# Kernel optimization log

Hardware: AMD Instinct MI355X
Metric: run time of the kernel (lower is better)

The kernel has to match this reference:

```python
import jax, jax.numpy as jnp
import numpy as np

VOCAB, EMB = 32000, 1024
HID, NLAYERS = 1024, 2
T, B, S = 64, 128, 128


def setup_inputs() -> dict:
    key = jax.random.key(0)
    ks = jax.random.split(key, 16)
    s = 1.0 / np.sqrt(HID)
    inp = {
        "input": jax.random.randint(ks[0], (T, B), 0, VOCAB),
        "h": jax.random.normal(ks[1], (NLAYERS, B, HID), jnp.float32),
        "H": jax.random.normal(ks[2], (S, B, HID), jnp.float32),
        "emb": jax.random.normal(ks[3], (VOCAB, EMB), jnp.float32) * 0.02,
        "w_ih": jax.random.uniform(ks[4], (NLAYERS, 3 * HID, EMB), jnp.float32, -s, s),
        "w_hh": jax.random.uniform(ks[5], (NLAYERS, 3 * HID, HID), jnp.float32, -s, s),
        "b_ih": jax.random.uniform(ks[6], (NLAYERS, 3 * HID), jnp.float32, -s, s),
        "b_hh": jax.random.uniform(ks[7], (NLAYERS, 3 * HID), jnp.float32, -s, s),
        "L1": jax.random.uniform(ks[8], (HID, HID), jnp.float32, -s, s),
        "L2": jax.random.uniform(ks[9], (HID, 2 * HID), jnp.float32, -s, s),
    }
    return inp


def _gru_cell(x, hprev, w_ih, w_hh, b_ih, b_hh):
    # x: (B, in), hprev: (B, HID); torch GRUCell gate order: r, z, n
    gi = x @ w_ih.T + b_ih          # (B, 3H)
    gh = hprev @ w_hh.T + b_hh      # (B, 3H)
    i_r, i_z, i_n = jnp.split(gi, 3, axis=-1)
    h_r, h_z, h_n = jnp.split(gh, 3, axis=-1)
    r = jax.nn.sigmoid(i_r + h_r)
    z = jax.nn.sigmoid(i_z + h_z)
    n = jnp.tanh(i_n + r * h_n)
    return (1.0 - z) * n + z * hprev


def reference(input, h, H, emb, w_ih, w_hh, b_ih, b_hh, L1, L2):
    embed = emb[input]                  # (T, B, EMB)
    Hc = jnp.transpose(H, (1, 0, 2))    # (B, S, HID)

    def step(hcarry, e):
        # stacked GRU cells
        hs = []
        o = e
        for i in range(NLAYERS):
            hi = _gru_cell(o, hcarry[i], w_ih[i], w_hh[i], b_ih[i], b_hh[i])
            hs.append(hi)
            o = hi
        hn = jnp.stack(hs)              # (L, B, HID)
        # global attention
        q1 = o @ L1.T                   # (B, HID)
        a = jax.nn.softmax(jnp.einsum('bsh,bh->bs', Hc, q1), axis=1)
        c = jnp.einsum('bs,bsh->bh', a, Hc)
        out = jnp.tanh(jnp.concatenate([c, o], axis=1) @ L2.T)
        return hn, out

    h_final, output = jax.lax.scan(step, h, embed)
    return output, h_final
```

## Files before the change

kernel.cpp:

```cpp
#include <hip/hip_runtime.h>

#define T_STEPS 64
#define BATCH   128
#define HID     1024
#define H3      3072
#define EMBD    1024
#define SLEN    128
#define BH      (BATCH * HID)

typedef __attribute__((ext_vector_type(8))) short short8;
typedef __attribute__((ext_vector_type(4))) float f32x4;

__device__ __forceinline__ unsigned short f2bf(float x) {
    unsigned int u = __float_as_uint(x);
    unsigned int r = (u + 0x7fffu + ((u >> 16) & 1u)) >> 16;
    return (unsigned short)r;
}
__device__ __forceinline__ float bf2f(unsigned short h) {
    return __uint_as_float(((unsigned int)h) << 16);
}
__device__ __forceinline__ unsigned int pk(unsigned short a, unsigned short b) {
    return (unsigned int)a | ((unsigned int)b << 16);
}
__device__ __forceinline__ void cvt8(const float4& x, const float4& y,
                                     uint4& H, uint4& L) {
    unsigned short h0 = f2bf(x.x), h1 = f2bf(x.y), h2 = f2bf(x.z), h3 = f2bf(x.w);
    unsigned short h4 = f2bf(y.x), h5 = f2bf(y.y), h6 = f2bf(y.z), h7 = f2bf(y.w);
    unsigned short l0 = f2bf(x.x - bf2f(h0)), l1 = f2bf(x.y - bf2f(h1));
    unsigned short l2 = f2bf(x.z - bf2f(h2)), l3 = f2bf(x.w - bf2f(h3));
    unsigned short l4 = f2bf(y.x - bf2f(h4)), l5 = f2bf(y.y - bf2f(h5));
    unsigned short l6 = f2bf(y.z - bf2f(h6)), l7 = f2bf(y.w - bf2f(h7));
    H = make_uint4(pk(h0,h1), pk(h2,h3), pk(h4,h5), pk(h6,h7));
    L = make_uint4(pk(l0,l1), pk(l2,l3), pk(l4,l5), pk(l6,l7));
}
__device__ __forceinline__ float sigf(float x) {
    return 1.f / (1.f + __expf(-x));
}

#define MF(A, B, ACC) ACC = __builtin_amdgcn_mfma_f32_16x16x32_bf16(A, B, ACC, 0, 0, 0)
#define TRI(AH, AL, WH, WL, ACC)  MF(AH, WL, ACC); MF(AL, WH, ACC); MF(AH, WH, ACC);

__global__ __launch_bounds__(256) void conv_planes_k(
    const float* __restrict__ src, short* __restrict__ hi, short* __restrict__ lo)
{
    const long i8 = (long)blockIdx.x * 256 + threadIdx.x;
    float4 x = ((const float4*)src)[i8 * 2];
    float4 y = ((const float4*)src)[i8 * 2 + 1];
    uint4 H, L; cvt8(x, y, H, L);
    ((uint4*)hi)[i8] = H; ((uint4*)lo)[i8] = L;
}

__global__ __launch_bounds__(256) void conv_cat_k(
    const float* __restrict__ wih1, const float* __restrict__ whh1,
    short* __restrict__ hi, short* __restrict__ lo)
{
    const long i8 = (long)blockIdx.x * 256 + threadIdx.x;
    const int k8 = (int)(i8 & 255);
    const long row = i8 >> 8;
    const int k = k8 * 8;
    const float* s = (k < 1024) ? (wih1 + row * 1024 + k) : (whh1 + row * 1024 + (k - 1024));
    float4 x = ((const float4*)s)[0];
    float4 y = ((const float4*)s)[1];
    uint4 H, L; cvt8(x, y, H, L);
    ((uint4*)hi)[i8] = H; ((uint4*)lo)[i8] = L;
}

__global__ __launch_bounds__(256) void conv_gather_k(
    const float* __restrict__ emb, const int* __restrict__ input,
    short* __restrict__ hi, short* __restrict__ lo)
{
    const long i8 = (long)blockIdx.x * 256 + threadIdx.x;
    const int c8 = (int)(i8 & 127);
    const long row = i8 >> 7;
    const float* s = emb + (size_t)input[row] * 1024 + c8 * 8;
    float4 x = ((const float4*)s)[0];
    float4 y = ((const float4*)s)[1];
    uint4 H, L; cvt8(x, y, H, L);
    ((uint4*)hi)[i8] = H; ((uint4*)lo)[i8] = L;
}

template<int MODE, bool CONCAT, bool WLO>
__global__ __launch_bounds__(256, 2) void gemm_big(
    const short* __restrict__ A1h, const short* __restrict__ A1l,
    const short* __restrict__ A2h, const short* __restrict__ A2l,
    const short* __restrict__ Wh,  const short* __restrict__ Wl,
    int K, int nn,
    const float* __restrict__ bias,
    float* __restrict__ outf, short* __restrict__ outh, short* __restrict__ outl,
    int ldo)
{
    extern __shared__ short sm[];
    short* Asm = sm;
    short* Wsm = sm + 16384;
    const int tid = threadIdx.x;
    const int wv = tid >> 6, l = tid & 63;
    const int mq = wv >> 1, nq = wv & 1;
    const int gl = l >> 4, r16 = l & 15;

    const int cpx = gridDim.x >> 3;
    const int id = blockIdx.x;
    const int swz = (id & 7) * cpx + (id >> 3);
    const int bm = swz / nn, bn = swz % nn;
    const long Rbase = (long)bm * 128;
    const int  Cbase = bn * 128;

    const int lda = CONCAT ? (K >> 1) : K;
    const int NC = K >> 5;
    const int NCh = NC >> 1;

    const short *aP1[4], *aP2[4], *wP[4];
    int slda[4];
    #pragma unroll
    for (int j = 0; j < 4; ++j) {
        const int s = tid + j * 256;
        const int pl = s >> 9, sp = s & 511;
        const int row = ((sp >> 6) << 4) | (sp & 15);
        const int kg = (sp >> 4) & 3;
        slda[j] = s * 8;
        const short* a1 = pl ? A1l : A1h;
        aP1[j] = a1 + (Rbase + row) * (long)lda + kg * 8;
        if (CONCAT) {
            const short* a2 = pl ? A2l : A2h;
            aP2[j] = a2 + (Rbase + row) * (long)lda + kg * 8;
        } else aP2[j] = aP1[j];
        const short* wp = pl ? Wl : Wh;
        wP[j] = wp + ((long)Cbase + row) * (long)K + kg * 8;
    }

    f32x4 acc[4][4];
    #pragma unroll
    for (int i = 0; i < 4; ++i)
        #pragma unroll
        for (int j = 0; j < 4; ++j) acc[i][j] = (f32x4)0.f;

    short8 rA[4], rW[4];
    auto LOADC = [&](int c) {
        const bool p1 = !CONCAT || (c < NCh);
        const long ko = p1 ? (long)c * 32 : (long)c * 32 - (K >> 1);
        #pragma unroll
        for (int j = 0; j < 4; ++j) {
            rA[j] = *(const short8*)((p1 ? aP1[j] : aP2[j]) + ko);
            rW[j] = *(const short8*)(wP[j] + (long)c * 32);
        }
    };
    auto STORE = [&](int c) {
        const int b = (c & 1) << 13;
        #pragma unroll
        for (int j = 0; j < 4; ++j) {
            *(short8*)(Asm + b + slda[j]) = rA[j];
            *(short8*)(Wsm + b + slda[j]) = rW[j];
        }
    };

    LOADC(0); STORE(0); LOADC(1);
    __syncthreads();

    for (int c = 0; c < NC; ++c) {
        const int b = (c & 1) << 13;
        short8 ah[4], al[4], wh[4], wl[4];
        #pragma unroll
        for (int f = 0; f < 4; ++f) {
            const short* ab = Asm + b + ((mq * 4 + f) * 64 + l) * 8;
            ah[f] = *(const short8*)ab;
            al[f] = *(const short8*)(ab + 4096);
            const short* wb = Wsm + b + ((nq * 4 + f) * 64 + l) * 8;
            wh[f] = *(const short8*)wb;
            if (!WLO) wl[f] = *(const short8*)(wb + 4096);
        }
        if (c + 1 < NC) STORE(c + 1);
        if (c + 2 < NC) LOADC(c + 2);
        #pragma unroll
        for (int mf = 0; mf < 4; ++mf)
            #pragma unroll
            for (int nf = 0; nf < 4; ++nf) {
                if constexpr (WLO) {
                    MF(al[mf], wh[nf], acc[mf][nf]);
                    MF(ah[mf], wh[nf], acc[mf][nf]);
                } else {
                    TRI(ah[mf], al[mf], wh[nf], wl[nf], acc[mf][nf]);
                }
            }
        __syncthreads();
    }

    #pragma unroll
    for (int mf = 0; mf < 4; ++mf) {
        #pragma unroll
        for (int reg = 0; reg < 4; ++reg) {
            const long R = Rbase + mq * 64 + mf * 16 + gl * 4 + reg;
            #pragma unroll
            for (int nf = 0; nf < 4; ++nf) {
                const int col = Cbase + nq * 64 + nf * 16 + r16;
                float v = acc[mf][nf][reg];
                if constexpr (MODE == 0) {
                    outf[R * (long)ldo + col] = v + bias[col];
                } else if constexpr (MODE == 1) {
                    const unsigned short hi = f2bf(v), lo = f2bf(v - bf2f(hi));
                    outh[R * (long)ldo + col] = (short)hi;
                    outl[R * (long)ldo + col] = (short)lo;
                } else {
                    outf[R * (long)ldo + col] = tanhf(v);
                }
            }
        }
    }
}

template<int MODE>
__device__ __forceinline__ void gru_core(
    int bm, int bj,
    const short* __restrict__ A1h, const short* __restrict__ A1l,
    const short* __restrict__ A2h, const short* __restrict__ A2l,
    const short* __restrict__ Wh,  const short* __restrict__ Wl,
    const float* __restrict__ bias, const float* __restrict__ bias2,
    const float* __restrict__ gi, const float* __restrict__ hprev,
    float* __restrict__ outf, short* __restrict__ outh, short* __restrict__ outl)
{
    extern __shared__ short sm[];
    constexpr int P = 3;
    constexpr int K = (MODE == 2) ? 1024 : 2048;
    constexpr int NC = K >> 6;
    constexpr int NCh = NC >> 1;
    const int ABUF = 8192, WBUF = P * 2048;
    short* Asm = sm;
    short* Wsm = sm + 2 * ABUF;
    const int tid = threadIdx.x;
    const int wv = tid >> 6, l = tid & 63;
    const int gl = l >> 4, r16 = l & 15;

    const short *a1hP[2], *a1lP[2], *a2hP[2], *a2lP[2];
    int aLds[2];
    #pragma unroll
    for (int i = 0; i < 2; ++i) {
        const int s = tid + i * 256;
        const int row = ((s >> 6) & 3) * 16 + (s & 15);
        const int kg  = ((s >> 8) << 2) | ((s >> 4) & 3);
        const long r = (long)bm * 64 + row;
        a1hP[i] = A1h + r * HID + kg * 8;
        a1lP[i] = A1l + r * HID + kg * 8;
        if (MODE == 3) {
            a2hP[i] = A2h + r * HID + kg * 8;
            a2lP[i] = A2l + r * HID + kg * 8;
        } else { a2hP[i] = a1hP[i]; a2lP[i] = a1lP[i]; }
        aLds[i] = s * 8;
    }
    const bool doW = tid < P * 64;
    const short *whP[2], *wlP[2];
    int wLds[2] = {0, 0};
    if (doW) {
        #pragma unroll
        for (int i = 0; i < 2; ++i) {
            const int s = tid + i * P * 64;
            const int kcw = s / (P * 64);
            const int rem = s - kcw * (P * 64);
            const int p = rem >> 6, ll = rem & 63;
            const int jr = ll & 15, g = ll >> 4;
            const int kg = kcw * 4 + g;
            const long grow = (long)(p << 10) + bj * 16 + jr;
            whP[i] = Wh + grow * (long)K + kg * 8;
            wlP[i] = Wl + grow * (long)K + kg * 8;
            wLds[i] = s * 8;
        }
    }

    constexpr int NACC = (MODE == 3) ? 4 : 3;
    f32x4 acc[NACC];
    #pragma unroll
    for (int i = 0; i < NACC; ++i) acc[i] = (f32x4)0.f;

    auto wloNeed = [&](int c) -> bool { return (MODE == 3) && (c < NCh); };

    short8 rAh[2], rAl[2], rWh[2], rWl[2];
    auto LOADC = [&](int c) {
        const bool part1 = (MODE == 2) || (c < NCh);
        const long ko = part1 ? (long)c * 64 : (long)c * 64 - (K >> 1);
        #pragma unroll
        for (int i = 0; i < 2; ++i) {
            rAh[i] = *(const short8*)((part1 ? a1hP[i] : a2hP[i]) + ko);
            rAl[i] = *(const short8*)((part1 ? a1lP[i] : a2lP[i]) + ko);
        }
        if (doW) {
            const bool wl = wloNeed(c);
            #pragma unroll
            for (int i = 0; i < 2; ++i) {
                rWh[i] = *(const short8*)(whP[i] + (long)c * 64);
                if (wl) rWl[i] = *(const short8*)(wlP[i] + (long)c * 64);
            }
        }
    };
    auto STORE = [&](int c) {
        const int b = c & 1;
        #pragma unroll
        for (int i = 0; i < 2; ++i) {
            *(short8*)(Asm + b * ABUF + aLds[i]) = rAh[i];
            *(short8*)(Asm + b * ABUF + 4096 + aLds[i]) = rAl[i];
        }
        if (doW) {
            const bool wl = wloNeed(c);
            #pragma unroll
            for (int i = 0; i < 2; ++i) {
                *(short8*)(Wsm + b * WBUF + wLds[i]) = rWh[i];
                if (wl) *(short8*)(Wsm + b * WBUF + P * 1024 + wLds[i]) = rWl[i];
            }
        }
    };

    LOADC(0); STORE(0); LOADC(1);
    __syncthreads();

    for (int c = 0; c < NC; ++c) {
        const int b = c & 1;
        const bool wl = wloNeed(c);
        short8 fah[2], fal[2], fwh[2][P], fwl[2][P];
        #pragma unroll
        for (int kc = 0; kc < 2; ++kc) {
            const short* ab = Asm + b * ABUF + (kc * 256 + wv * 64 + l) * 8;
            fah[kc] = *(const short8*)ab;
            fal[kc] = *(const short8*)(ab + 4096);
            #pragma unroll
            for (int p = 0; p < P; ++p) {
                const short* wb = Wsm + b * WBUF + (kc * (P * 64) + p * 64 + l) * 8;
                fwh[kc][p] = *(const short8*)wb;
                if (wl) fwl[kc][p] = *(const short8*)(wb + P * 1024);
            }
        }
        if (c + 1 < NC) STORE(c + 1);
        if (c + 2 < NC) LOADC(c + 2);
        #pragma unroll
        for (int kc = 0; kc < 2; ++kc) {
            if constexpr (MODE == 3) {
                if (c < NCh) {
                    TRI(fah[kc], fal[kc], fwh[kc][0], fwl[kc][0], acc[0]);
                    TRI(fah[kc], fal[kc], fwh[kc][1], fwl[kc][1], acc[1]);
                    TRI(fah[kc], fal[kc], fwh[kc][2], fwl[kc][2], acc[2]);
                } else {
                    MF(fal[kc], fwh[kc][0], acc[0]); MF(fah[kc], fwh[kc][0], acc[0]);
                    MF(fal[kc], fwh[kc][1], acc[1]); MF(fah[kc], fwh[kc][1], acc[1]);
                    MF(fal[kc], fwh[kc][2], acc[3]); MF(fah[kc], fwh[kc][2], acc[3]);
                }
            } else {
                #pragma unroll
                for (int p = 0; p < P; ++p) {
                    MF(fal[kc], fwh[kc][p], acc[p]); MF(fah[kc], fwh[kc][p], acc[p]);
                }
            }
        }
        __syncthreads();
    }

    const int jc = bj * 16 + r16;
    #pragma unroll
    for (int reg = 0; reg < 4; ++reg) {
        const long R = (long)bm * 64 + wv * 16 + gl * 4 + reg;
        float h;
        if constexpr (MODE == 2) {
            const float* orow = gi + R * H3;
            const float rr = sigf(orow[jc] + acc[0][reg] + bias[jc]);
            const float zz = sigf(orow[HID + jc] + acc[1][reg] + bias[HID + jc]);
            const float nn = tanhf(orow[2 * HID + jc] + rr * (acc[2][reg] + bias[2 * HID + jc]));
            h = (1.f - zz) * nn + zz * hprev[R * HID + jc];
        } else {
            const float rr = sigf(acc[0][reg] + bias[jc] + bias2[jc]);
            const float zz = sigf(acc[1][reg] + bias[HID + jc] + bias2[HID + jc]);
            const float nn = tanhf(acc[2][reg] + bias[2 * HID + jc] +
                                   rr * (acc[3][reg] + bias2[2 * HID + jc]));
            h = (1.f - zz) * nn + zz * hprev[R * HID + jc];
        }
        outf[R * HID + jc] = h;
        const unsigned short hb = f2bf(h), lb = f2bf(h - bf2f(hb));
        outh[R * HID + jc] = (short)hb;
        outl[R * HID + jc] = (short)lb;
    }
}

struct StepP {
    const short* hih; const short* hil;
    const float* h_in; const float* gi0;
    const short* whh0h;
    const short* wcath; const short* wcatl;
    const float* b_hh0; const float* b_ih1; const float* b_hh1;
    float* h0f; float* h1f;
    short* h0ah; short* h0al; short* h1ah; short* h1al;
};

__global__ __launch_bounds__(256) void step_k(int t, StepP P)
{
    const int id = blockIdx.x;
    const int xcd = id & 7, sub = (id >> 3) & 7, top = id >> 6;
    const int role = top >> 1, bm = top & 1;
    const int bj = xcd * 8 + sub;

    if (role == 0) {
        if (t >= T_STEPS) return;
        const short* a1h = t ? P.h0ah + (size_t)(t - 1) * BH : P.hih;
        const short* a1l = t ? P.h0al + (size_t)(t - 1) * BH : P.hil;
        gru_core<2>(bm, bj, a1h, a1l, nullptr, nullptr,
                    P.whh0h, nullptr, P.b_hh0, nullptr,
                    P.gi0 + (size_t)t * BATCH * H3,
                    t ? P.h0f + (size_t)((t - 1) & 1) * BH : P.h_in,
                    P.h0f + (size_t)(t & 1) * BH,
                    P.h0ah + (size_t)t * BH, P.h0al + (size_t)t * BH);
    } else {
        if (t < 1) return;
        const int s = t - 1;
        const short* a2h = s ? P.h1ah + (size_t)(s - 1) * BH : P.hih + BH;
        const short* a2l = s ? P.h1al + (size_t)(s - 1) * BH : P.hil + BH;
        gru_core<3>(bm, bj,
                    P.h0ah + (size_t)s * BH, P.h0al + (size_t)s * BH, a2h, a2l,
                    P.wcath, P.wcatl, P.b_ih1, P.b_hh1,
                    nullptr,
                    s ? P.h1f + (size_t)((s - 1) & 1) * BH : P.h_in + BH,
                    P.h1f + (size_t)(s & 1) * BH,
                    P.h1ah + (size_t)s * BH, P.h1al + (size_t)s * BH);
    }
}

__global__ __launch_bounds__(256) void scores_k(
    const short* __restrict__ Qh, const short* __restrict__ Ql,
    const short* __restrict__ Hh, const short* __restrict__ Hl,
    float* __restrict__ Pall)
{
    extern __shared__ short sm[];
    short* Asm = sm;
    short* Wsm = sm + 8192;
    const int b = blockIdx.x, tid = threadIdx.x;
    const int wv = tid >> 6, l = tid & 63;
    const int gl = l >> 4, cc = l & 15;

    const int arow = ((tid >> 6) & 3) * 16 + (tid & 15);
    const int ag   = (tid >> 4) & 3;
    const short* qhp = Qh + ((long)arow * BATCH + b) * HID + ag * 8;
    const short* qlp = Ql + ((long)arow * BATCH + b) * HID + ag * 8;
    const int aLds = tid * 8;

    const short *whp[2], *wlp[2]; int wLds[2];
    #pragma unroll
    for (int i = 0; i < 2; ++i) {
        const int s = tid + i * 256;
        const int srow = ((s >> 6) & 7) * 16 + (s & 15);
        const int sg   = (s >> 4) & 3;
        whp[i] = Hh + ((long)srow * BATCH + b) * HID + sg * 8;
        wlp[i] = Hl + ((long)srow * BATCH + b) * HID + sg * 8;
        wLds[i] = s * 8;
    }

    f32x4 acc[8];
    #pragma unroll
    for (int i = 0; i < 8; ++i) acc[i] = (f32x4)0.f;

    short8 rAh, rAl, rWh[2], rWl[2];
    auto LOADC = [&](int c) {
        rAh = *(const short8*)(qhp + c * 32);
        rAl = *(const short8*)(qlp + c * 32);
        #pragma unroll
        for (int i = 0; i < 2; ++i) {
            rWh[i] = *(const short8*)(whp[i] + c * 32);
            rWl[i] = *(const short8*)(wlp[i] + c * 32);
        }
    };
    auto STORE = [&](int c) {
        const int bb = c & 1;
        *(short8*)(Asm + bb * 4096 + aLds) = rAh;
        *(short8*)(Asm + bb * 4096 + 2048 + aLds) = rAl;
        #pragma unroll
        for (int i = 0; i < 2; ++i) {
            *(short8*)(Wsm + bb * 8192 + wLds[i]) = rWh[i];
            *(short8*)(Wsm + bb * 8192 + 4096 + wLds[i]) = rWl[i];
        }
    };

    LOADC(0); STORE(0); LOADC(1);
    __syncthreads();
    for (int c = 0; c < 32; ++c) {
        const int bb = c & 1;
        const short* abp = Asm + bb * 4096 + (wv * 64 + l) * 8;
        short8 ah = *(const short8*)abp;
        short8 al = *(const short8*)(abp + 2048);
        if (c + 1 < 32) STORE(c + 1);
        if (c + 2 < 32) LOADC(c + 2);
        #pragma unroll
        for (int jt = 0; jt < 8; ++jt) {
            const short* wbp = Wsm + bb * 8192 + (jt * 64 + l) * 8;
            short8 wh = *(const short8*)wbp;
            short8 wl = *(const short8*)(wbp + 4096);
            TRI(ah, al, wh, wl, acc[jt]);
        }
        __syncthreads();
    }

    #pragma unroll
    for (int reg = 0; reg < 4; ++reg) {
        float m = acc[0][reg];
        #pragma unroll
        for (int jt = 1; jt < 8; ++jt) m = fmaxf(m, acc[jt][reg]);
        #pragma unroll
        for (int off = 1; off < 16; off <<= 1) m = fmaxf(m, __shfl_xor(m, off));
        float e[8], ssum = 0.f;
        #pragma unroll
        for (int jt = 0; jt < 8; ++jt) { e[jt] = __expf(acc[jt][reg] - m); ssum += e[jt]; }
        #pragma unroll
        for (int off = 1; off < 16; off <<= 1) ssum += __shfl_xor(ssum, off);
        const float inv = 1.f / ssum;
        const int t = wv * 16 + gl * 4 + reg;
        #pragma unroll
        for (int jt = 0; jt < 8; ++jt)
            Pall[((long)t * BATCH + b) * SLEN + jt * 16 + cc] = e[jt] * inv;
    }
}

__global__ __launch_bounds__(256) void ctx_k(
    const float* __restrict__ Pall, const float* __restrict__ H,
    short* __restrict__ Ch, short* __restrict__ Cl)
{
    __shared__ float Ps[T_STEPS * SLEN];
    const int b = blockIdx.x, ht = blockIdx.y, tid = threadIdx.x;
    for (int i = 0; i < 32; ++i) {
        const int idx = i * 256 + tid;
        const int t = idx >> 7, s = idx & 127;
        Ps[idx] = Pall[((long)t * BATCH + b) * SLEN + s];
    }
    __syncthreads();
    const int col = ht * 256 + tid;
    for (int tg = 0; tg < 4; ++tg) {
        float a[16];
        #pragma unroll
        for (int j = 0; j < 16; ++j) a[j] = 0.f;
        for (int s = 0; s < SLEN; ++s) {
            const float hv = H[((long)s * BATCH + b) * HID + col];
            #pragma unroll
            for (int j = 0; j < 16; ++j)
                a[j] = fmaf(Ps[(tg * 16 + j) * SLEN + s], hv, a[j]);
        }
        #pragma unroll
        for (int j = 0; j < 16; ++j) {
            const long row = (long)(tg * 16 + j) * BATCH + b;
            const unsigned short hi = f2bf(a[j]);
            const unsigned short lo = f2bf(a[j] - bf2f(hi));
            Ch[row * HID + col] = (short)hi;
            Cl[row * HID + col] = (short)lo;
        }
    }
}

extern "C" void kernel_launch(void* const* d_in, const int* in_sizes, int n_in,
                              void* d_out, int out_size, void* d_ws, size_t ws_size,
                              hipStream_t stream)
{
    const int*   input = (const int*)  d_in[0];
    const float* h_in  = (const float*)d_in[1];
    const float* Hbuf  = (const float*)d_in[2];
    const float* emb   = (const float*)d_in[3];
    const float* w_ih  = (const float*)d_in[4];
    const float* w_hh  = (const float*)d_in[5];
    const float* b_ih  = (const float*)d_in[6];
    const float* b_hh  = (const float*)d_in[7];
    const float* L1    = (const float*)d_in[8];
    const float* L2    = (const float*)d_in[9];

    float* out = (float*)d_out;

    char* basep = (char*)d_ws;
    size_t off = 0;
    auto alloc = [&](size_t bytes) -> char* {
        off = (off + 255) & ~(size_t)255;
        char* p = basep + off; off += bytes; return p;
    };
    short* wih0h = (short*)alloc(3072L*1024*2); short* wih0l = (short*)alloc(3072L*1024*2);
    short* whh0h = (short*)alloc(3072L*1024*2); short* whh0l = (short*)alloc(3072L*1024*2);
    short* wcath = (short*)alloc(3072L*2048*2); short* wcatl = (short*)alloc(3072L*2048*2);
    short* l1h   = (short*)alloc(1024L*1024*2); short* l1l   = (short*)alloc(1024L*1024*2);
    short* l2h   = (short*)alloc(1024L*2048*2); short* l2l   = (short*)alloc(1024L*2048*2);
    short* Hh    = (short*)alloc(16777216L*2);  short* Hl    = (short*)alloc(16777216L*2);
    short* hih   = (short*)alloc(262144L*2);    short* hil   = (short*)alloc(262144L*2);
    short* h0ah  = (short*)alloc(8388608L*2);   short* h0al  = (short*)alloc(8388608L*2);
    short* h1ah  = (short*)alloc(8388608L*2);   short* h1al  = (short*)alloc(8388608L*2);
    short* eqh   = (short*)alloc(8388608L*2);   short* eql   = (short*)alloc(8388608L*2);
    float* gi0   = (float*)alloc(25165824L*4);
    float* h0f   = (float*)alloc(524288L*4);
    float* h1f   = (float*)alloc(524288L*4);
    float* Pall  = (float*)alloc(1048576L*4);
    short* ctxh  = (short*)gi0;
    short* ctxl  = ctxh + 8388608L;

    const dim3 blk(256);
    const size_t SMB = 32768 * sizeof(short);
    const size_t SM3 = (2 * 8192 + 2 * 3 * 2048) * sizeof(short);

    conv_planes_k<<<1536, blk, 0, stream>>>(w_ih, wih0h, wih0l);
    conv_planes_k<<<1536, blk, 0, stream>>>(w_hh, whh0h, whh0l);
    conv_cat_k<<<3072, blk, 0, stream>>>(w_ih + (size_t)H3 * EMBD,
                                         w_hh + (size_t)H3 * HID, wcath, wcatl);
    conv_planes_k<<<512,  blk, 0, stream>>>(L1, l1h, l1l);
    conv_planes_k<<<1024, blk, 0, stream>>>(L2, l2h, l2l);
    conv_planes_k<<<8192, blk, 0, stream>>>(Hbuf, Hh, Hl);
    conv_planes_k<<<128,  blk, 0, stream>>>(h_in, hih, hil);
    conv_gather_k<<<4096, blk, 0, stream>>>(emb, input, eqh, eql);

    gemm_big<0, false, true><<<dim3(1536), blk, SMB, stream>>>(
        eqh, eql, nullptr, nullptr, wih0h, wih0l, 1024, 24,
        b_ih, gi0, nullptr, nullptr, H3);

    StepP sp;
    sp.hih = hih; sp.hil = hil; sp.h_in = h_in; sp.gi0 = gi0;
    sp.whh0h = whh0h; sp.wcath = wcath; sp.wcatl = wcatl;
    sp.b_hh0 = b_hh; sp.b_ih1 = b_ih + H3; sp.b_hh1 = b_hh + H3;
    sp.h0f = h0f; sp.h1f = h1f;
    sp.h0ah = h0ah; sp.h0al = h0al; sp.h1ah = h1ah; sp.h1al = h1al;
    for (int t = 0; t <= T_STEPS; ++t)
        step_k<<<dim3(256), blk, SM3, stream>>>(t, sp);

    gemm_big<1, false, false><<<dim3(512), blk, SMB, stream>>>(
        h1ah, h1al, nullptr, nullptr, l1h, l1l, 1024, 8,
        nullptr, nullptr, eqh, eql, HID);
    scores_k<<<dim3(BATCH), blk, 49152, stream>>>(eqh, eql, Hh, Hl, Pall);
    ctx_k<<<dim3(BATCH, 4), blk, 0, stream>>>(Pall, Hbuf, ctxh, ctxl);
    gemm_big<2, true, false><<<dim3(512), blk, SMB, stream>>>(
        ctxh, ctxl, h1ah, h1al, l2h, l2l, 2048, 8,
        nullptr, out, nullptr, nullptr, HID);

    hipMemcpyAsync(out + (long)T_STEPS * BH, h0f + BH, (size_t)BH * 4,
                   hipMemcpyDeviceToDevice, stream);
    hipMemcpyAsync(out + (long)T_STEPS * BH + BH, h1f + BH, (size_t)BH * 4,
                   hipMemcpyDeviceToDevice, stream);
}
```

Measured before the change: 2.233 ms.

## Split layer-1 GRU into separate input and recurrent stages in a three-phase pipeline

```diff
diff --git a/kernel.cpp b/kernel.cpp
--- a/kernel.cpp
+++ b/kernel.cpp
@@ -46,21 +46,6 @@
     const long i8 = (long)blockIdx.x * 256 + threadIdx.x;
     float4 x = ((const float4*)src)[i8 * 2];
     float4 y = ((const float4*)src)[i8 * 2 + 1];
-    uint4 H, L; cvt8(x, y, H, L);
-    ((uint4*)hi)[i8] = H; ((uint4*)lo)[i8] = L;
-}
-
-__global__ __launch_bounds__(256) void conv_cat_k(
-    const float* __restrict__ wih1, const float* __restrict__ whh1,
-    short* __restrict__ hi, short* __restrict__ lo)
-{
-    const long i8 = (long)blockIdx.x * 256 + threadIdx.x;
-    const int k8 = (int)(i8 & 255);
-    const long row = i8 >> 8;
-    const int k = k8 * 8;
-    const float* s = (k < 1024) ? (wih1 + row * 1024 + k) : (whh1 + row * 1024 + (k - 1024));
-    float4 x = ((const float4*)s)[0];
-    float4 y = ((const float4*)s)[1];
     uint4 H, L; cvt8(x, y, H, L);
     ((uint4*)hi)[i8] = H; ((uint4*)lo)[i8] = L;
 }
@@ -209,18 +194,17 @@
 template<int MODE>
 __device__ __forceinline__ void gru_core(
     int bm, int bj,
-    const short* __restrict__ A1h, const short* __restrict__ A1l,
-    const short* __restrict__ A2h, const short* __restrict__ A2l,
+    const short* __restrict__ Ah, const short* __restrict__ Al,
     const short* __restrict__ Wh,  const short* __restrict__ Wl,
-    const float* __restrict__ bias, const float* __restrict__ bias2,
+    const float* __restrict__ bias,
     const float* __restrict__ gi, const float* __restrict__ hprev,
-    float* __restrict__ outf, short* __restrict__ outh, short* __restrict__ outl)
+    float* __restrict__ outf,
+    short* __restrict__ outh, short* __restrict__ outl)
 {
     extern __shared__ short sm[];
     constexpr int P = 3;
-    constexpr int K = (MODE == 2) ? 1024 : 2048;
-    constexpr int NC = K >> 6;
-    constexpr int NCh = NC >> 1;
+    constexpr int NC = 16;
+    constexpr bool WL = (MODE == 0);
     const int ABUF = 8192, WBUF = P * 2048;
     short* Asm = sm;
     short* Wsm = sm + 2 * ABUF;
@@ -228,7 +212,7 @@
     const int wv = tid >> 6, l = tid & 63;
     const int gl = l >> 4, r16 = l & 15;
 
-    const short *a1hP[2], *a1lP[2], *a2hP[2], *a2lP[2];
+    const short *ahP[2], *alP[2];
     int aLds[2];
     #pragma unroll
     for (int i = 0; i < 2; ++i) {
@@ -236,12 +220,8 @@
         const int row = ((s >> 6) & 3) * 16 + (s & 15);
         const int kg  = ((s >> 8) << 2) | ((s >> 4) & 3);
         const long r = (long)bm * 64 + row;
-        a1hP[i] = A1h + r * HID + kg * 8;
-        a1lP[i] = A1l + r * HID + kg * 8;
-        if (MODE == 3) {
-            a2hP[i] = A2h + r * HID + kg * 8;
-            a2lP[i] = A2l + r * HID + kg * 8;
-        } else { a2hP[i] = a1hP[i]; a2lP[i] = a1lP[i]; }
+        ahP[i] = Ah + r * HID + kg * 8;
+        alP[i] = Al + r * HID + kg * 8;
         aLds[i] = s * 8;
     }
     const bool doW = tid < P * 64;
@@ -257,34 +237,29 @@
             const int jr = ll & 15, g = ll >> 4;
             const int kg = kcw * 4 + g;
             const long grow = (long)(p << 10) + bj * 16 + jr;
-            whP[i] = Wh + grow * (long)K + kg * 8;
-            wlP[i] = Wl + grow * (long)K + kg * 8;
+            whP[i] = Wh + grow * (long)HID + kg * 8;
+            wlP[i] = WL ? Wl + grow * (long)HID + kg * 8 : whP[i];
             wLds[i] = s * 8;
         }
     }
 
-    constexpr int NACC = (MODE == 3) ? 4 : 3;
-    f32x4 acc[NACC];
-    #pragma unroll
-    for (int i = 0; i < NACC; ++i) acc[i] = (f32x4)0.f;
-
-    auto wloNeed = [&](int c) -> bool { return (MODE == 3) && (c < NCh); };
+    f32x4 acc[P];
+    #pragma unroll
+    for (int i = 0; i < P; ++i) acc[i] = (f32x4)0.f;
 
     short8 rAh[2], rAl[2], rWh[2], rWl[2];
     auto LOADC = [&](int c) {
-        const bool part1 = (MODE == 2) || (c < NCh);
-        const long ko = part1 ? (long)c * 64 : (long)c * 64 - (K >> 1);
+        const long ko = (long)c * 64;
         #pragma unroll
         for (int i = 0; i < 2; ++i) {
-            rAh[i] = *(const short8*)((part1 ? a1hP[i] : a2hP[i]) + ko);
-            rAl[i] = *(const short8*)((part1 ? a1lP[i] : a2lP[i]) + ko);
+            rAh[i] = *(const short8*)(ahP[i] + ko);
+            rAl[i] = *(const short8*)(alP[i] + ko);
         }
         if (doW) {
-            const bool wl = wloNeed(c);
             #pragma unroll
             for (int i = 0; i < 2; ++i) {
-                rWh[i] = *(const short8*)(whP[i] + (long)c * 64);
-                if (wl) rWl[i] = *(const short8*)(wlP[i] + (long)c * 64);
+                rWh[i] = *(const short8*)(whP[i] + ko);
+                if (WL) rWl[i] = *(const short8*)(wlP[i] + ko);
             }
         }
     };
@@ -296,11 +271,10 @@
             *(short8*)(Asm + b * ABUF + 4096 + aLds[i]) = rAl[i];
         }
         if (doW) {
-            const bool wl = wloNeed(c);
             #pragma unroll
             for (int i = 0; i < 2; ++i) {
                 *(short8*)(Wsm + b * WBUF + wLds[i]) = rWh[i];
-                if (wl) *(short8*)(Wsm + b * WBUF + P * 1024 + wLds[i]) = rWl[i];
+                if (WL) *(short8*)(Wsm + b * WBUF + P * 1024 + wLds[i]) = rWl[i];
             }
         }
     };
@@ -310,7 +284,6 @@
 
     for (int c = 0; c < NC; ++c) {
         const int b = c & 1;
-        const bool wl = wloNeed(c);
         short8 fah[2], fal[2], fwh[2][P], fwl[2][P];
         #pragma unroll
         for (int kc = 0; kc < 2; ++kc) {
@@ -321,27 +294,20 @@
             for (int p = 0; p < P; ++p) {
                 const short* wb = Wsm + b * WBUF + (kc * (P * 64) + p * 64 + l) * 8;
                 fwh[kc][p] = *(const short8*)wb;
-                if (wl) fwl[kc][p] = *(const short8*)(wb + P * 1024);
+                if (WL) fwl[kc][p] = *(const short8*)(wb + P * 1024);
             }
         }
         if (c + 1 < NC) STORE(c + 1);
         if (c + 2 < NC) LOADC(c + 2);
         #pragma unroll
         for (int kc = 0; kc < 2; ++kc) {
-            if constexpr (MODE == 3) {
-                if (c < NCh) {
-                    TRI(fah[kc], fal[kc], fwh[kc][0], fwl[kc][0], acc[0]);
-                    TRI(fah[kc], fal[kc], fwh[kc][1], fwl[kc][1], acc[1]);
-                    TRI(fah[kc], fal[kc], fwh[kc][2], fwl[kc][2], acc[2]);
+            #pragma unroll
+            for (int p = 0; p < P; ++p) {
+                if constexpr (MODE == 0) {
+                    TRI(fah[kc], fal[kc], fwh[kc][p], fwl[kc][p], acc[p]);
                 } else {
-                    MF(fal[kc], fwh[kc][0], acc[0]); MF(fah[kc], fwh[kc][0], acc[0]);
-                    MF(fal[kc], fwh[kc][1], acc[1]); MF(fah[kc], fwh[kc][1], acc[1]);
-                    MF(fal[kc], fwh[kc][2], acc[3]); MF(fah[kc], fwh[kc][2], acc[3]);
-                }
-            } else {
-                #pragma unroll
-                for (int p = 0; p < P; ++p) {
-                    MF(fal[kc], fwh[kc][p], acc[p]); MF(fah[kc], fwh[kc][p], acc[p]);
+                    MF(fal[kc], fwh[kc][p], acc[p]);
+                    MF(fah[kc], fwh[kc][p], acc[p]);
                 }
             }
         }
@@ -352,38 +318,35 @@
     #pragma unroll
     for (int reg = 0; reg < 4; ++reg) {
         const long R = (long)bm * 64 + wv * 16 + gl * 4 + reg;
-        float h;
-        if constexpr (MODE == 2) {
+        if constexpr (MODE == 0) {
+            #pragma unroll
+            for (int p = 0; p < P; ++p)
+                outf[R * H3 + p * HID + jc] = acc[p][reg] + bias[p * HID + jc];
+        } else {
             const float* orow = gi + R * H3;
             const float rr = sigf(orow[jc] + acc[0][reg] + bias[jc]);
             const float zz = sigf(orow[HID + jc] + acc[1][reg] + bias[HID + jc]);
             const float nn = tanhf(orow[2 * HID + jc] + rr * (acc[2][reg] + bias[2 * HID + jc]));
-            h = (1.f - zz) * nn + zz * hprev[R * HID + jc];
-        } else {
-            const float rr = sigf(acc[0][reg] + bias[jc] + bias2[jc]);
-            const float zz = sigf(acc[1][reg] + bias[HID + jc] + bias2[HID + jc]);
-            const float nn = tanhf(acc[2][reg] + bias[2 * HID + jc] +
-                                   rr * (acc[3][reg] + bias2[2 * HID + jc]));
-            h = (1.f - zz) * nn + zz * hprev[R * HID + jc];
-        }
-        outf[R * HID + jc] = h;
-        const unsigned short hb = f2bf(h), lb = f2bf(h - bf2f(hb));
-        outh[R * HID + jc] = (short)hb;
-        outl[R * HID + jc] = (short)lb;
+            const float h = (1.f - zz) * nn + zz * hprev[R * HID + jc];
+            outf[R * HID + jc] = h;
+            const unsigned short hb = f2bf(h), lb = f2bf(h - bf2f(hb));
+            outh[R * HID + jc] = (short)hb;
+            outl[R * HID + jc] = (short)lb;
+        }
     }
 }
 
 struct StepP {
     const short* hih; const short* hil;
-    const float* h_in; const float* gi0;
+    const float* h_in; const float* gi0; float* gi1;
     const short* whh0h;
-    const short* wcath; const short* wcatl;
+    const short* wih1h; const short* wih1l; const short* whh1h;
     const float* b_hh0; const float* b_ih1; const float* b_hh1;
     float* h0f; float* h1f;
     short* h0ah; short* h0al; short* h1ah; short* h1al;
 };
 
-__global__ __launch_bounds__(256) void step_k(int t, StepP P)
+__global__ __launch_bounds__(256) void step_k(int ph, StepP P)
 {
     const int id = blockIdx.x;
     const int xcd = id & 7, sub = (id >> 3) & 7, top = id >> 6;
@@ -391,24 +354,31 @@
     const int bj = xcd * 8 + sub;
 
     if (role == 0) {
+        const int t = ph;
         if (t >= T_STEPS) return;
         const short* a1h = t ? P.h0ah + (size_t)(t - 1) * BH : P.hih;
         const short* a1l = t ? P.h0al + (size_t)(t - 1) * BH : P.hil;
-        gru_core<2>(bm, bj, a1h, a1l, nullptr, nullptr,
-                    P.whh0h, nullptr, P.b_hh0, nullptr,
+        gru_core<2>(bm, bj, a1h, a1l, P.whh0h, nullptr, P.b_hh0,
                     P.gi0 + (size_t)t * BATCH * H3,
                     t ? P.h0f + (size_t)((t - 1) & 1) * BH : P.h_in,
                     P.h0f + (size_t)(t & 1) * BH,
                     P.h0ah + (size_t)t * BH, P.h0al + (size_t)t * BH);
+    } else if (role == 1) {
+        const int s = ph - 1;
+        if (s < 0 || s >= T_STEPS) return;
+        gru_core<0>(bm, bj,
+                    P.h0ah + (size_t)s * BH, P.h0al + (size_t)s * BH,
+                    P.wih1h, P.wih1l, P.b_ih1,
+                    nullptr, nullptr,
+                    P.gi1 + (size_t)(s & 1) * BATCH * H3,
+                    nullptr, nullptr);
     } else {
-        if (t < 1) return;
-        const int s = t - 1;
-        const short* a2h = s ? P.h1ah + (size_t)(s - 1) * BH : P.hih + BH;
-        const short* a2l = s ? P.h1al + (size_t)(s - 1) * BH : P.hil + BH;
-        gru_core<3>(bm, bj,
-                    P.h0ah + (size_t)s * BH, P.h0al + (size_t)s * BH, a2h, a2l,
-                    P.wcath, P.wcatl, P.b_ih1, P.b_hh1,
-                    nullptr,
+        const int s = ph - 2;
+        if (s < 0 || s >= T_STEPS) return;
+        const short* a1h = s ? P.h1ah + (size_t)(s - 1) * BH : P.hih + BH;
+        const short* a1l = s ? P.h1al + (size_t)(s - 1) * BH : P.hil + BH;
+        gru_core<2>(bm, bj, a1h, a1l, P.whh1h, nullptr, P.b_hh1,
+                    P.gi1 + (size_t)(s & 1) * BATCH * H3,
                     s ? P.h1f + (size_t)((s - 1) & 1) * BH : P.h_in + BH,
                     P.h1f + (size_t)(s & 1) * BH,
                     P.h1ah + (size_t)s * BH, P.h1al + (size_t)s * BH);
@@ -567,7 +537,8 @@
     };
     short* wih0h = (short*)alloc(3072L*1024*2); short* wih0l = (short*)alloc(3072L*1024*2);
     short* whh0h = (short*)alloc(3072L*1024*2); short* whh0l = (short*)alloc(3072L*1024*2);
-    short* wcath = (short*)alloc(3072L*2048*2); short* wcatl = (short*)alloc(3072L*2048*2);
+    short* wih1h = (short*)alloc(3072L*1024*2); short* wih1l = (short*)alloc(3072L*1024*2);
+    short* whh1h = (short*)alloc(3072L*1024*2); short* whh1l = (short*)alloc(3072L*1024*2);
     short* l1h   = (short*)alloc(1024L*1024*2); short* l1l   = (short*)alloc(1024L*1024*2);
     short* l2h   = (short*)alloc(1024L*2048*2); short* l2l   = (short*)alloc(1024L*2048*2);
     short* Hh    = (short*)alloc(16777216L*2);  short* Hl    = (short*)alloc(16777216L*2);
@@ -576,6 +547,7 @@
     short* h1ah  = (short*)alloc(8388608L*2);   short* h1al  = (short*)alloc(8388608L*2);
     short* eqh   = (short*)alloc(8388608L*2);   short* eql   = (short*)alloc(8388608L*2);
     float* gi0   = (float*)alloc(25165824L*4);
+    float* gi1   = (float*)alloc(2L*BATCH*H3*4);
     float* h0f   = (float*)alloc(524288L*4);
     float* h1f   = (float*)alloc(524288L*4);
     float* Pall  = (float*)alloc(1048576L*4);
@@ -588,8 +560,8 @@
 
     conv_planes_k<<<1536, blk, 0, stream>>>(w_ih, wih0h, wih0l);
     conv_planes_k<<<1536, blk, 0, stream>>>(w_hh, whh0h, whh0l);
-    conv_cat_k<<<3072, blk, 0, stream>>>(w_ih + (size_t)H3 * EMBD,
-                                         w_hh + (size_t)H3 * HID, wcath, wcatl);
+    conv_planes_k<<<1536, blk, 0, stream>>>(w_ih + 3145728L, wih1h, wih1l);
+    conv_planes_k<<<1536, blk, 0, stream>>>(w_hh + 3145728L, whh1h, whh1l);
     conv_planes_k<<<512,  blk, 0, stream>>>(L1, l1h, l1l);
     conv_planes_k<<<1024, blk, 0, stream>>>(L2, l2h, l2l);
     conv_planes_k<<<8192, blk, 0, stream>>>(Hbuf, Hh, Hl);
@@ -601,13 +573,14 @@
         b_ih, gi0, nullptr, nullptr, H3);
 
     StepP sp;
-    sp.hih = hih; sp.hil = hil; sp.h_in = h_in; sp.gi0 = gi0;
-    sp.whh0h = whh0h; sp.wcath = wcath; sp.wcatl = wcatl;
+    sp.hih = hih; sp.hil = hil; sp.h_in = h_in; sp.gi0 = gi0; sp.gi1 = gi1;
+    sp.whh0h = whh0h;
+    sp.wih1h = wih1h; sp.wih1l = wih1l; sp.whh1h = whh1h;
     sp.b_hh0 = b_hh; sp.b_ih1 = b_ih + H3; sp.b_hh1 = b_hh + H3;
     sp.h0f = h0f; sp.h1f = h1f;
     sp.h0ah = h0ah; sp.h0al = h0al; sp.h1ah = h1ah; sp.h1al = h1al;
-    for (int t = 0; t <= T_STEPS; ++t)
-        step_k<<<dim3(256), blk, SM3, stream>>>(t, sp);
+    for (int ph = 0; ph <= T_STEPS + 1; ++ph)
+        step_k<<<dim3(384), blk, SM3, stream>>>(ph, sp);
 
     gemm_big<1, false, false><<<dim3(512), blk, SMB, stream>>>(
         h1ah, h1al, nullptr, nullptr, l1h, l1l, 1024, 8,
```

Measured after the change: 2.105 ms. -5.7%, faster.
